# Optimization experiments

Hardware: AMD Instinct MI355X
Metric: run time of the kernel (lower is better)

The kernel has to match this reference:

```python
import jax, jax.numpy as jnp
import numpy as np

SPLINE_DEG = 3      # cubic B-spline basis (Cox-de Boor)
SPAN_FACTOR = 0.1   # module default span_factor


def _bspline_basis(x, knots):
    """Vectorized Cox-de Boor. x: (N, D) clamped into knot support; knots: (D, M).
    Returns basis (N, D, M - 1 - SPLINE_DEG)."""
    t = knots[None, :, :]                                   # (1, D, M)
    xe = x[..., None]                                        # (N, D, 1)
    B = ((xe >= t[..., :-1]) & (xe < t[..., 1:])).astype(x.dtype)
    for d in range(1, SPLINE_DEG + 1):
        den_l = t[..., d:-1] - t[..., :-(d + 1)]
        den_r = t[..., d + 1:] - t[..., 1:-d]
        wl = (xe - t[..., :-(d + 1)]) / jnp.where(den_l > 0, den_l, jnp.ones_like(den_l))
        wr = (t[..., d + 1:] - xe) / jnp.where(den_r > 0, den_r, jnp.ones_like(den_r))
        B = wl * B[..., :-1] + wr * B[..., 1:]
    return B


def setup_inputs() -> dict:
    key = jax.random.key(0)
    k1, k2 = jax.random.split(key)
    N, D, degree = 262144, 16, 10
    L = D * (D - 1) // 2                                     # 120 pairwise lambdas
    inp = jax.random.normal(k1, (N, D), dtype=jnp.float32)
    # module initializes all coeffs to 0.1; add tiny noise for non-degenerate math
    params = 0.1 + 0.01 * jax.random.normal(k2, (degree + 1, L), dtype=jnp.float32)
    polynomial_range = jnp.stack([-5.0 * jnp.ones(D, jnp.float32),
                                   5.0 * jnp.ones(D, jnp.float32)])  # (2, D)
    return {"input": inp, "params": params, "polynomial_range": polynomial_range}


def reference(input, params, polynomial_range):
    N, D = input.shape
    K = params.shape[0]                                      # degree + 1 basis funcs
    low0, high0 = polynomial_range[0], polynomial_range[1]   # (D,), (D,)
    span = high0 - low0
    low = low0 - SPAN_FACTOR * span
    high = high0 + SPAN_FACTOR * span
    n_seg = K - SPLINE_DEG                                   # interior segments
    h = (high - low) / n_seg                                 # (D,)
    i = jnp.arange(-SPLINE_DEG, K + 1, dtype=input.dtype)    # M = K + SPLINE_DEG + 1 knots
    knots = low[:, None] + i[None, :] * h[:, None]           # (D, M)
    eps = 1e-6 * (high - low)
    xc = jnp.clip(input, low[None, :], (high - eps)[None, :])
    B = _bspline_basis(xc, knots)                            # (N, D, K)

    # static pair bookkeeping: params_index order is (v, c) for v in range(D), c < v
    var_idx, cov_idx = [], []
    for v in range(D):
        for c in range(v):
            var_idx.append(v); cov_idx.append(c)
    var_idx = np.asarray(var_idx); cov_idx = np.asarray(cov_idx)

    # P[c, k, v] = params[k, pair(v, c)]; zero where no pair (c >= v)
    Pmat = jnp.zeros((D, K, D), dtype=params.dtype).at[cov_idx, :, var_idx].set(params.T)
    # output[:, v] = input[:, v] + sum_{c<v} (B[:, c, :] @ params[:, pair]) * input[:, c]
    out = input + jnp.einsum('nck,ckv,nc->nv', B, Pmat, input)

    # P-spline ridge penalties, summed over all L pair coefficient vectors
    d1 = params[1:] - params[:-1]
    d2 = params[2:] - 2.0 * params[1:-1] + params[:-2]
    second_order_pen = jnp.sum(d2 ** 2)
    first_order_pen = jnp.sum(d1 ** 2)
    param_pen = jnp.sum(params ** 2)
    return out, second_order_pen, first_order_pen, param_pen
```

## Files before the change

kernel.cpp:

```cpp
#include <hip/hip_runtime.h>
#include <hip/hip_bf16.h>


constexpr int D    = 16;
constexpr int K    = 11;
constexpr int L    = 120;
constexpr int NSEG = 8;
constexpr int SEG_STRIDE = L * 4 + 4;

__global__ __launch_bounds__(256) void decor_fused(
    const float* __restrict__ x, const float* __restrict__ params,
    const float* __restrict__ prange, float* __restrict__ out, int N) {
  __shared__ float T[NSEG * SEG_STRIDE];

  for (int idx = threadIdx.x; idx < NSEG * L; idx += 256) {
    int s = idx / L;
    int l = idx - s * L;
    float p0 = params[(s + 0) * L + l];
    float p1 = params[(s + 1) * L + l];
    float p2 = params[(s + 2) * L + l];
    float p3 = params[(s + 3) * L + l];
    float* c = &T[s * SEG_STRIDE + l * 4];
    c[0] = (p0 + 4.0f * p1 + p2) * (1.0f / 6.0f);
    c[1] = (p2 - p0) * 0.5f;
    c[2] = (p0 - 2.0f * p1 + p2) * 0.5f;
    c[3] = (p3 - p0) * (1.0f / 6.0f) + (p1 - p2) * 0.5f;
  }

  if (blockIdx.x == 0) {
    float s2 = 0.0f, s1 = 0.0f, s0 = 0.0f;
    for (int i = threadIdx.x; i < (K - 2) * L; i += 256) {
      float v = params[i + 2 * L] - 2.0f * params[i + L] + params[i];
      s2 += v * v;
    }
    for (int i = threadIdx.x; i < (K - 1) * L; i += 256) {
      float v = params[i + L] - params[i];
      s1 += v * v;
    }
    for (int i = threadIdx.x; i < K * L; i += 256) {
      float v = params[i];
      s0 += v * v;
    }
#pragma unroll
    for (int off = 32; off > 0; off >>= 1) {
      s2 += __shfl_down(s2, off);
      s1 += __shfl_down(s1, off);
      s0 += __shfl_down(s0, off);
    }
    __shared__ float r[3][4];
    int wid = threadIdx.x >> 6, lane = threadIdx.x & 63;
    if (lane == 0) { r[0][wid] = s2; r[1][wid] = s1; r[2][wid] = s0; }
    __syncthreads();
    if (threadIdx.x == 0) {
      float* o = out + (size_t)N * D;
      o[0] = r[0][0] + r[0][1] + r[0][2] + r[0][3];
      o[1] = r[1][0] + r[1][1] + r[1][2] + r[1][3];
      o[2] = r[2][0] + r[2][1] + r[2][2] + r[2][3];
    }
  }
  __syncthreads();

  int n = blockIdx.x * 256 + threadIdx.x;
  if (n >= N) return;

  float xv[D];
  const float4* xr = reinterpret_cast<const float4*>(x + (size_t)n * D);
#pragma unroll
  for (int i = 0; i < D / 4; ++i) {
    float4 v = xr[i];
    xv[4 * i + 0] = v.x; xv[4 * i + 1] = v.y;
    xv[4 * i + 2] = v.z; xv[4 * i + 3] = v.w;
  }

  float u[D];
  int   sb[D];
#pragma unroll
  for (int d = 0; d < D; ++d) {
    float lo0  = prange[d];
    float hi0  = prange[D + d];
    float span = hi0 - lo0;
    float lo   = lo0 - 0.1f * span;
    float hi   = hi0 + 0.1f * span;
    float eps  = 1e-6f * (hi - lo);
    float hinv = (float)NSEG / (hi - lo);
    float xc   = fminf(fmaxf(xv[d], lo), hi - eps);
    float t    = (xc - lo) * hinv;
    int   s    = (int)t;
    s          = s > NSEG - 1 ? NSEG - 1 : s;
    u[d]       = t - (float)s;
    sb[d]      = s * (SEG_STRIDE * 4);
  }

  float acc[D];
#pragma unroll
  for (int v = 0; v < D; ++v) acc[v] = xv[v];

  const char* Tb = reinterpret_cast<const char*>(T);
#pragma unroll
  for (int v = 1; v < D; ++v) {
    const int lbase = v * (v - 1) / 2;
#pragma unroll
    for (int c = 0; c < v; ++c) {
      const float4 cf =
          *reinterpret_cast<const float4*>(Tb + sb[c] + (lbase + c) * 16);
      float q = fmaf(fmaf(fmaf(cf.w, u[c], cf.z), u[c], cf.y), u[c], cf.x);
      acc[v] = fmaf(q, xv[c], acc[v]);
    }
  }

  float4* orow = reinterpret_cast<float4*>(out + (size_t)n * D);
#pragma unroll
  for (int i = 0; i < D / 4; ++i) {
    orow[i] = make_float4(acc[4 * i + 0], acc[4 * i + 1],
                          acc[4 * i + 2], acc[4 * i + 3]);
  }
}

extern "C" void kernel_launch(void* const* d_in, const int* in_sizes, int n_in,
                              void* d_out, int out_size, void* d_ws,
                              size_t ws_size, hipStream_t stream) {
  const float* x      = (const float*)d_in[0];
  const float* params = (const float*)d_in[1];
  const float* prange = (const float*)d_in[2];
  float* out = (float*)d_out;
  int N = in_sizes[0] / D;

  int blocks = (N + 255) / 256;
  decor_fused<<<blocks, 256, 0, stream>>>(x, params, prange, out, N);
}
```

Measured before the change: 83.12 us.

## Split coefficient table build into pre-kernel and serve odd pairs from global memory

Adds a single-block pre-kernel that writes the cubic coefficient table to workspace and computes the penalty sums, which removes the block-0 special path from the main kernel. The main kernel still builds the table in LDS, but now loads odd-indexed pair coefficients from the global (cached) copy and even ones from LDS. The intent is to spread the per-row gather traffic across the LDS and vector-cache paths to ease LDS bandwidth pressure. It costs an extra kernel launch and serialisation between the two kernels, and the global loads are data-dependent gathers whose latency may exceed that of LDS.

```diff
diff --git a/kernel.cpp b/kernel.cpp
--- a/kernel.cpp
+++ b/kernel.cpp
@@ -8,55 +8,70 @@
 constexpr int NSEG = 8;
 constexpr int SEG_STRIDE = L * 4 + 4;
 
-__global__ __launch_bounds__(256) void decor_fused(
+__device__ __forceinline__ void coef(const float* __restrict__ p, int s, int l,
+                                     float4* c) {
+  float p0 = p[(s + 0) * L + l];
+  float p1 = p[(s + 1) * L + l];
+  float p2 = p[(s + 2) * L + l];
+  float p3 = p[(s + 3) * L + l];
+  c->x = (p0 + 4.0f * p1 + p2) * (1.0f / 6.0f);
+  c->y = (p2 - p0) * 0.5f;
+  c->z = (p0 - 2.0f * p1 + p2) * 0.5f;
+  c->w = (p3 - p0) * (1.0f / 6.0f) + (p1 - p2) * 0.5f;
+}
+
+__global__ __launch_bounds__(256) void build_and_pen(
+    const float* __restrict__ params, float* __restrict__ gT,
+    float* __restrict__ pen_out) {
+  for (int idx = threadIdx.x; idx < NSEG * L; idx += 256) {
+    int s = idx / L;
+    int l = idx - s * L;
+    float4 c;
+    coef(params, s, l, &c);
+    *reinterpret_cast<float4*>(&gT[s * SEG_STRIDE + l * 4]) = c;
+  }
+  float s2 = 0.0f, s1 = 0.0f, s0 = 0.0f;
+  for (int i = threadIdx.x; i < (K - 2) * L; i += 256) {
+    float v = params[i + 2 * L] - 2.0f * params[i + L] + params[i];
+    s2 += v * v;
+  }
+  for (int i = threadIdx.x; i < (K - 1) * L; i += 256) {
+    float v = params[i + L] - params[i];
+    s1 += v * v;
+  }
+  for (int i = threadIdx.x; i < K * L; i += 256) {
+    float v = params[i];
+    s0 += v * v;
+  }
+#pragma unroll
+  for (int off = 32; off > 0; off >>= 1) {
+    s2 += __shfl_down(s2, off);
+    s1 += __shfl_down(s1, off);
+    s0 += __shfl_down(s0, off);
+  }
+  __shared__ float r[3][4];
+  int wid = threadIdx.x >> 6, lane = threadIdx.x & 63;
+  if (lane == 0) { r[0][wid] = s2; r[1][wid] = s1; r[2][wid] = s0; }
+  __syncthreads();
+  if (threadIdx.x == 0) {
+    pen_out[0] = r[0][0] + r[0][1] + r[0][2] + r[0][3];
+    pen_out[1] = r[1][0] + r[1][1] + r[1][2] + r[1][3];
+    pen_out[2] = r[2][0] + r[2][1] + r[2][2] + r[2][3];
+  }
+}
+
+__global__ __launch_bounds__(256) void decor_kernel(
     const float* __restrict__ x, const float* __restrict__ params,
-    const float* __restrict__ prange, float* __restrict__ out, int N) {
+    const float* __restrict__ prange, const float* __restrict__ gT,
+    float* __restrict__ out, int N) {
   __shared__ float T[NSEG * SEG_STRIDE];
 
   for (int idx = threadIdx.x; idx < NSEG * L; idx += 256) {
     int s = idx / L;
     int l = idx - s * L;
-    float p0 = params[(s + 0) * L + l];
-    float p1 = params[(s + 1) * L + l];
-    float p2 = params[(s + 2) * L + l];
-    float p3 = params[(s + 3) * L + l];
-    float* c = &T[s * SEG_STRIDE + l * 4];
-    c[0] = (p0 + 4.0f * p1 + p2) * (1.0f / 6.0f);
-    c[1] = (p2 - p0) * 0.5f;
-    c[2] = (p0 - 2.0f * p1 + p2) * 0.5f;
-    c[3] = (p3 - p0) * (1.0f / 6.0f) + (p1 - p2) * 0.5f;
-  }
-
-  if (blockIdx.x == 0) {
-    float s2 = 0.0f, s1 = 0.0f, s0 = 0.0f;
-    for (int i = threadIdx.x; i < (K - 2) * L; i += 256) {
-      float v = params[i + 2 * L] - 2.0f * params[i + L] + params[i];
-      s2 += v * v;
-    }
-    for (int i = threadIdx.x; i < (K - 1) * L; i += 256) {
-      float v = params[i + L] - params[i];
-      s1 += v * v;
-    }
-    for (int i = threadIdx.x; i < K * L; i += 256) {
-      float v = params[i];
-      s0 += v * v;
-    }
-#pragma unroll
-    for (int off = 32; off > 0; off >>= 1) {
-      s2 += __shfl_down(s2, off);
-      s1 += __shfl_down(s1, off);
-      s0 += __shfl_down(s0, off);
-    }
-    __shared__ float r[3][4];
-    int wid = threadIdx.x >> 6, lane = threadIdx.x & 63;
-    if (lane == 0) { r[0][wid] = s2; r[1][wid] = s1; r[2][wid] = s0; }
-    __syncthreads();
-    if (threadIdx.x == 0) {
-      float* o = out + (size_t)N * D;
-      o[0] = r[0][0] + r[0][1] + r[0][2] + r[0][3];
-      o[1] = r[1][0] + r[1][1] + r[1][2] + r[1][3];
-      o[2] = r[2][0] + r[2][1] + r[2][2] + r[2][3];
-    }
+    float4 c;
+    coef(params, s, l, &c);
+    *reinterpret_cast<float4*>(&T[s * SEG_STRIDE + l * 4]) = c;
   }
   __syncthreads();
 
@@ -96,13 +111,16 @@
   for (int v = 0; v < D; ++v) acc[v] = xv[v];
 
   const char* Tb = reinterpret_cast<const char*>(T);
+  const char* Gb = reinterpret_cast<const char*>(gT);
 #pragma unroll
   for (int v = 1; v < D; ++v) {
     const int lbase = v * (v - 1) / 2;
 #pragma unroll
     for (int c = 0; c < v; ++c) {
+      const int l = lbase + c;
       const float4 cf =
-          *reinterpret_cast<const float4*>(Tb + sb[c] + (lbase + c) * 16);
+          (l & 1) ? *reinterpret_cast<const float4*>(Gb + sb[c] + l * 16)
+                  : *reinterpret_cast<const float4*>(Tb + sb[c] + l * 16);
       float q = fmaf(fmaf(fmaf(cf.w, u[c], cf.z), u[c], cf.y), u[c], cf.x);
       acc[v] = fmaf(q, xv[c], acc[v]);
     }
@@ -123,8 +141,10 @@
   const float* params = (const float*)d_in[1];
   const float* prange = (const float*)d_in[2];
   float* out = (float*)d_out;
+  float* gT  = (float*)d_ws;
   int N = in_sizes[0] / D;
 
+  build_and_pen<<<1, 256, 0, stream>>>(params, gT, out + (size_t)N * D);
   int blocks = (N + 255) / 256;
-  decor_fused<<<blocks, 256, 0, stream>>>(x, params, prange, out, N);
+  decor_kernel<<<blocks, 256, 0, stream>>>(x, params, prange, gT, out, N);
 }
```

Result: slower. 92.83 us (+11.7%).
